# Optimization experiments

Measured on AMD Instinct MI355X. Metric: run time of the kernel, lower is better.

Reference implementation:

```python
import jax, jax.numpy as jnp
import numpy as np

M, D, NI, L, NPL, R, T = 2, 128, 131072, 4, 2048, 8, 32
N = NI + L * NPL  # total DAG nodes


def setup_inputs() -> dict:
    key = jax.random.key(0)
    ks = jax.random.split(key, 18)
    thax = jax.random.randint(ks[0], (NI,), 0, T)
    sine = jax.random.uniform(ks[1], (NI,), jnp.float32)
    # parents of layer-l deriv nodes index any node built earlier (topological)
    raw = jax.random.randint(ks[2], (L, NPL, 2), 0, 2**30)
    bounds = jnp.array([NI + l * NPL for l in range(L)])[:, None, None]
    par = raw % bounds
    ridx = jax.random.randint(ks[3], (L, NPL), 0, R)
    pos = jax.random.uniform(ks[4], (N,), jnp.float32) + 0.01
    neg = jax.random.uniform(ks[5], (N,), jnp.float32) + 0.01
    s = 0.05
    return {
        'thax': thax, 'sine': sine, 'par': par, 'ridx': ridx,
        'pos': pos, 'neg': neg,
        'init_table': jax.random.normal(ks[6], (M, T, D)) * s,
        's_vec': jax.random.normal(ks[7], (M, D)) * s,
        'W1': jax.random.normal(ks[8], (M, R, 2 * D, D)) * s,
        'b1': jax.random.normal(ks[9], (M, R, D)) * s,
        'W2': jax.random.normal(ks[10], (M, R, D, D)) * s,
        'b2': jax.random.normal(ks[11], (M, R, D)) * s,
        'tweaks': jax.random.normal(ks[12], (M, 1, 2)) * s,
        'We1': jax.random.normal(ks[13], (M, D, D)) * s,
        'be1': jax.random.normal(ks[14], (M, D)) * s,
        'we2': jax.random.normal(ks[15], (M, D)) * s,
        'be2': jax.random.normal(ks[16], (M,)) * s,
    }


def reference(thax, sine, par, ridx, pos, neg, init_table, s_vec,
              W1, b1, W2, b2, tweaks, We1, be1, we2, be2):
    # init nodes: thax embedding + sine embellishment (per model)
    emb0 = init_table[:, thax, :] + sine[None, :, None] * s_vec[:, None, :]  # [M,NI,D]
    store = jnp.zeros((M, N, D), emb0.dtype).at[:, :NI].set(emb0)
    # topological layers of deriv nodes: gather parents, rule-indexed 2-layer MLP
    for l in range(L):
        p, r = par[l], ridx[l]
        cat = store[:, p].reshape(M, NPL, 2 * D)               # gather parents
        h = jax.nn.relu(jnp.einsum('mnc,mncd->mnd', cat, W1[:, r]) + b1[:, r])
        out = (jnp.einsum('mnd,mnde->mne', h, W2[:, r]) + b2[:, r]
               + tweaks[:, 0, 1][:, None, None])
        store = store.at[:, NI + l * NPL: NI + (l + 1) * NPL].set(out)
    # eval_net: per-node scalar logit (+ per-problem tweak)
    he = jax.nn.relu(jnp.einsum('mnd,mde->mne', store, We1) + be1[:, None, :])
    logit = jnp.einsum('mnd,md->mn', he, we2) + be2[:, None] + tweaks[:, 0, 0][:, None]
    tot_pos, tot_neg = pos.sum(), neg.sum()
    pw = tot_neg / tot_pos  # POS_WEIGHT_EXTRA = 1.0
    gold = pos / (pos + neg)
    w = pos + neg
    # BCEWithLogitsLoss(pos_weight=pw) per node, weighted by (pos+neg)
    bce = -(pw * gold[None] * jax.nn.log_sigmoid(logit)
            + (1.0 - gold[None]) * jax.nn.log_sigmoid(-logit))
    loss = (w[None] * bce).sum(axis=1)                          # [M]
    posOK = jnp.where(logit >= 0, pos[None], 0.0).sum(axis=1)
    negOK = jnp.where(logit < 0, neg[None], 0.0).sum(axis=1)
    return (loss, posOK, negOK, tot_pos, tot_neg)
```

## Files before the change

kernel.cpp:

```cpp
#include <hip/hip_runtime.h>
#include <hip/hip_bf16.h>

#define M_ 2
#define D_ 128
#define NI_ 131072
#define L_ 4
#define NPL_ 2048
#define R_ 8
#define T_ 32
#define N_ (NI_ + L_ * NPL_)
#define ND_ (L_ * NPL_)
#define PSTRIDE_ 1792
#define PUSED_ 1665
#define FCAP_ 1280
#define SCAP_ 512
#define CCAP_ 24

typedef __bf16 bf16x8 __attribute__((ext_vector_type(8)));
typedef float f32x4 __attribute__((ext_vector_type(4)));
typedef unsigned short u16x4 __attribute__((ext_vector_type(4)));

#define OFF_W2T    0u
#define OFF_WE1T   524288u
#define OFF_TAB    589824u
#define OFF_SVEC   606208u
#define OFF_EA2    606720u
#define OFF_EWB    639488u
#define OFF_PA     641536u
#define OFF_PB     655872u
#define OFF_PPOK   670208u
#define OFF_PNOK   684544u
#define OFF_PTP    698880u
#define OFF_PTN    706048u
#define OFF_G      713216u
#define OFF_FLIST  1253888u
#define OFF_SLIST  1294848u
#define OFF_CFG    1296896u

__device__ __forceinline__ unsigned short f2bu(float f) {
  unsigned int u = __float_as_uint(f);
  u += 0x7fffu + ((u >> 16) & 1u);
  return (unsigned short)(u >> 16);
}
__device__ __forceinline__ float bfu2f(unsigned short u) {
  return __uint_as_float((unsigned int)u << 16);
}
__device__ __forceinline__ bf16x8 ldb8(const unsigned short* p) {
  return *reinterpret_cast<const bf16x8*>(p);
}

__global__ __launch_bounds__(256) void megaprep_kernel(
    const float* W1, const float* W2, const float* We1,
    const float* init_table, const float* s_vec,
    const float* b1, const float* be1, const float* we2,
    const int* ridx, const int* par,
    unsigned short* W2T, unsigned short* We1T,
    unsigned short* tab, unsigned short* svec,
    float* G, float* EA2, float* EWB,
    int* fastlist, int* slowlist, int* cfg, unsigned int* pzero) {
  __shared__ float smem[4352];
  __shared__ int lcnt;
  int job = blockIdx.x;
  int tid = threadIdx.x;

  if (job < 9) {
    int* out; int cap;
    if (job < 8) { out = fastlist + job * FCAP_; cap = FCAP_; }
    else         { out = slowlist;               cap = SCAP_; }
    if (tid == 0) lcnt = 0;
    __syncthreads();
    int lane = tid & 63;
    unsigned long long lmask_lt = (1ull << lane) - 1ull;
    for (int g = tid; g < ND_; g += 256) {
      int p0 = par[2 * g], p1 = par[2 * g + 1];
      bool fast = (p0 < NI_) && (p1 < NI_);
      bool match = (job < 8) ? (fast && ridx[g] == job) : (!fast);
      unsigned long long mask = __ballot(match);
      if (mask) {
        int leader = __ffsll((unsigned long long)mask) - 1;
        int pre = __popcll(mask & lmask_lt);
        int base_ = 0;
        if (lane == leader) base_ = atomicAdd(&lcnt, __popcll(mask));
        base_ = __shfl(base_, leader, 64);
        if (match) {
          int idx = base_ + pre;
          if (idx < cap) out[idx] = g;
        }
      }
    }
    __syncthreads();
    if (tid == 0) {
      int c = lcnt; if (c > cap) c = cap;
      cfg[job] = c;
    }
  } else if (job < 41) {
    int q = job - 9;
    int mr = q >> 1, slot = q & 1;
    int m = mr >> 3;
    for (int i = tid; i < 4352; i += 256) {
      int t = i >> 7, c = i & 127;
      smem[i] = (t < 32) ? init_table[(size_t)(m * T_ + t) * D_ + c]
              : (t == 32) ? s_vec[(size_t)m * D_ + c] : 0.f;
    }
    __syncthreads();
    int e = tid & 127, tg = tid >> 7;
    int t0 = tg ? 17 : 0;
    int nt = tg ? 16 : 17;
    float acc[17];
#pragma unroll
    for (int k = 0; k < 17; ++k) acc[k] = 0.f;
    const float* w1base = &W1[(size_t)(mr * 256 + slot * 128) * D_ + e];
#pragma unroll 4
    for (int c = 0; c < 128; ++c) {
      float w1c = w1base[(size_t)c * D_];
#pragma unroll
      for (int k = 0; k < 17; ++k)
        acc[k] = fmaf(smem[(t0 + k) * 128 + c], w1c, acc[k]);
    }
    float bb = b1[mr * D_ + e];
    for (int k = 0; k < nt; ++k) {
      int t = t0 + k;
      float v = acc[k];
      if (slot == 0 && t < 32) v += bb;
      G[((size_t)(mr * 2 + slot) * 33 + t) * D_ + e] = v;
    }
  } else if (job < 43) {
    int m = job - 41;
    for (int i = tid; i < 4352; i += 256) {
      int t = i >> 7, c = i & 127;
      smem[i] = (t < 32) ? init_table[(size_t)(m * T_ + t) * D_ + c]
              : (t == 32) ? s_vec[(size_t)m * D_ + c] : 0.f;
    }
    __syncthreads();
    int e = tid & 127, tg = tid >> 7;
    int t0 = tg ? 17 : 0;
    int nt = tg ? 16 : 17;
    float acc[17];
#pragma unroll
    for (int k = 0; k < 17; ++k) acc[k] = 0.f;
    const float* webase = &We1[(size_t)m * D_ * D_ + e];
#pragma unroll 4
    for (int c = 0; c < 128; ++c) {
      float wc = webase[(size_t)c * D_];
#pragma unroll
      for (int k = 0; k < 17; ++k)
        acc[k] = fmaf(smem[(t0 + k) * 128 + c], wc, acc[k]);
    }
    float bev = be1[m * D_ + e];
    for (int k = 0; k < nt; ++k) {
      int t = t0 + k;
      if (t < 32) {
        EA2[m * 4096 + ((e >> 1) * 32 + t) * 2 + (e & 1)] = acc[k] + bev;
      } else {
        EWB[(m * D_ + e) * 2 + 0] = acc[k];
        EWB[(m * D_ + e) * 2 + 1] = we2[m * D_ + e];
      }
    }
  } else if (job == 43) {
    for (int i = tid; i < 17920; i += 256) pzero[i] = 0u;
  } else if (job == 44) {
    for (int i = tid; i < 8448; i += 256) {
      if (i < 8192) tab[i] = f2bu(init_table[i]);
      else svec[i - 8192] = f2bu(s_vec[i - 8192]);
    }
  } else {
    int q0 = job - 45;
    const float* src; unsigned short* dst;
    int rblk, cblk;
    if (q0 < 256) {
      int z = q0 >> 4;
      src = W2 + (size_t)z * 16384; dst = W2T + (size_t)z * 16384;
      rblk = (q0 & 15) >> 2; cblk = q0 & 3;
    } else {
      int q = q0 - 256; int z = q >> 4;
      src = We1 + (size_t)z * 16384; dst = We1T + (size_t)z * 16384;
      rblk = (q & 15) >> 2; cblk = q & 3;
    }
    int r0 = rblk * 32, c0 = cblk * 32;
    float (*tile)[33] = (float(*)[33])smem;
    int tx = tid & 31, ty = tid >> 5;
#pragma unroll
    for (int k = 0; k < 4; ++k)
      tile[ty + 8 * k][tx] = src[(size_t)(r0 + ty + 8 * k) * D_ + c0 + tx];
    __syncthreads();
#pragma unroll
    for (int k = 0; k < 4; ++k)
      dst[(size_t)(c0 + ty + 8 * k) * D_ + r0 + tx] = f2bu(tile[tx][ty + 8 * k]);
  }
}

__global__ __launch_bounds__(256) void main_kernel(
    const int* thax, const float* sine, const int* par, const int* ridx,
    const float* pos, const float* neg,
    const float* W1, const float* b1, const float* b2, const float* tweaks,
    const float* G, const unsigned short* W2T, const unsigned short* We1T,
    const unsigned short* tab, const unsigned short* svec,
    const float* EA2, const float* EWB,
    const float* be1, const float* we2, const float* be2,
    const int* cfg, const int* fastlist, const int* slowlist,
    float* pA, float* pB, float* pPok, float* pNok, float* pTp, float* pTn) {
  __shared__ float sbuf[4448];
  int bid = blockIdx.x;
  int tid = threadIdx.x;
  int w = tid >> 6, lane = tid & 63;

  if (bid < 1024) {
    int m = bid >> 9, si = bid & 511;
    if (si >= cfg[8]) return;
    int*   list  = (int*)sbuf;
    int*   meta  = (int*)(sbuf + 24);
    unsigned short* catl = (unsigned short*)(sbuf + 32);
    float* hbuf  = sbuf + 160;
    float* hp0   = sbuf + 288;
    float* hp1   = sbuf + 416;
    unsigned short* cache = (unsigned short*)(sbuf + 544);

    int g_row = slowlist[si];
    if (tid == 0) {
      int nn = 0;
      list[nn++] = g_row;
      for (int i = 0; i < nn; ++i) {
        int g = list[i];
        for (int s = 0; s < 2; ++s) {
          int p = par[2 * g + s];
          if (p >= NI_) {
            int pg = p - NI_;
            bool found = false;
            for (int jj = 0; jj < nn; ++jj) if (list[jj] == pg) { found = true; break; }
            if (!found && nn < CCAP_) list[nn++] = pg;
          }
        }
      }
      for (int i = 1; i < nn; ++i) {
        int v = list[i]; int jj = i - 1;
        while (jj >= 0 && list[jj] > v) { list[jj + 1] = list[jj]; --jj; }
        list[jj + 1] = v;
      }
      meta[0] = nn;
    }
    __syncthreads();
    int NN = meta[0];
    float tw1 = tweaks[m * 2 + 1];
    for (int j = 0; j < NN; ++j) {
      int g = list[j];
      int r = ridx[g];
      int p0 = par[2 * g], p1 = par[2 * g + 1];
      bool fastn = (p0 < NI_) && (p1 < NI_);
      if (fastn) {
        if (tid < 128) {
          int d = tid;
          const float* Gm = &G[(size_t)(m * R_ + r) * 8448];
          float hv = Gm[thax[p0] * 128 + d] + Gm[(33 + thax[p1]) * 128 + d]
                   + sine[p0] * Gm[4096 + d] + sine[p1] * Gm[8320 + d];
          hbuf[d] = bfu2f(f2bu(fmaxf(hv, 0.f)));
        }
        __syncthreads();
      } else {
        if (tid == 0) {
          int s0 = -1, s1 = -1;
          if (p0 >= NI_) for (int jj = 0; jj < j; ++jj) if (list[jj] == p0 - NI_) { s0 = jj; break; }
          if (p1 >= NI_) for (int jj = 0; jj < j; ++jj) if (list[jj] == p1 - NI_) { s1 = jj; break; }
          meta[1] = s0; meta[2] = s1;
        }
        __syncthreads();
        {
          int c = tid; int p = (c < 128) ? p0 : p1; int cc = c & 127;
          int slot = (c < 128) ? meta[1] : meta[2];
          unsigned short v;
          if (p < NI_) {
            float tv = bfu2f(tab[(m * T_ + thax[p]) * D_ + cc])
                     + sine[p] * bfu2f(svec[m * D_ + cc]);
            v = f2bu(tv);
          } else {
            v = cache[slot * 128 + cc];
          }
          catl[c] = v;
        }
        __syncthreads();
        int d = tid & 127, half = tid >> 7;
        const float* w1r = &W1[(((size_t)(m * R_ + r)) * 256 + half * 128) * D_];
        float acc = 0.f;
#pragma unroll 8
        for (int c = 0; c < 128; ++c)
          acc = fmaf(bfu2f(catl[half * 128 + c]), w1r[(size_t)c * D_ + d], acc);
        if (half == 0) hp0[d] = acc; else hp1[d] = acc;
        __syncthreads();
        if (tid < 128) {
          float hv = b1[(m * R_ + r) * D_ + tid] + hp0[tid] + hp1[tid];
          hbuf[tid] = bfu2f(f2bu(fmaxf(hv, 0.f)));
        }
        __syncthreads();
      }
      {
        int e = tid & 127, half = tid >> 7;
        const u16x4* w2r4 = (const u16x4*)&W2T[((size_t)(m * R_ + r) * D_ + e) * D_ + half * 64];
        float acc = 0.f;
#pragma unroll
        for (int dd = 0; dd < 16; ++dd) {
          u16x4 wv = w2r4[dd];
          int db = half * 64 + dd * 4;
          acc = fmaf(bfu2f(wv[0]), hbuf[db + 0], acc);
          acc = fmaf(bfu2f(wv[1]), hbuf[db + 1], acc);
          acc = fmaf(bfu2f(wv[2]), hbuf[db + 2], acc);
          acc = fmaf(bfu2f(wv[3]), hbuf[db + 3], acc);
        }
        if (half == 0) hp0[e] = acc; else hp1[e] = acc;
      }
      __syncthreads();
      if (tid < 128) {
        float o = hp0[tid] + hp1[tid] + b2[(m * R_ + r) * D_ + tid] + tw1;
        cache[j * 128 + tid] = f2bu(o);
      }
      __syncthreads();
    }
    int jr = NN - 1;
    {
      int e = tid & 127, half = tid >> 7;
      const u16x4* wer4 = (const u16x4*)&We1T[((size_t)m * D_ + e) * D_ + half * 64];
      float acc = 0.f;
#pragma unroll
      for (int dd = 0; dd < 16; ++dd) {
        u16x4 wv = wer4[dd];
        int db = half * 64 + dd * 4;
        acc = fmaf(bfu2f(wv[0]), bfu2f(cache[jr * 128 + db + 0]), acc);
        acc = fmaf(bfu2f(wv[1]), bfu2f(cache[jr * 128 + db + 1]), acc);
        acc = fmaf(bfu2f(wv[2]), bfu2f(cache[jr * 128 + db + 2]), acc);
        acc = fmaf(bfu2f(wv[3]), bfu2f(cache[jr * 128 + db + 3]), acc);
      }
      if (half == 0) hp0[e] = acc; else hp1[e] = acc;
    }
    __syncthreads();
    if (tid < 128) {
      float he = hp0[tid] + hp1[tid] + be1[m * D_ + tid];
      he = he > 0.f ? he : 0.f;
      hbuf[tid] = he * we2[m * D_ + tid];
    }
    __syncthreads();
    if (tid < 64) {
      float s = hbuf[tid] + hbuf[tid + 64];
#pragma unroll
      for (int mask = 1; mask < 64; mask <<= 1) s += __shfl_xor(s, mask, 64);
      if (tid == 0) {
        float logit = s + be2[m] + tweaks[m * 2 + 0];
        int grow = NI_ + g_row;
        float p_ = pos[grow], n_ = neg[grow];
        float lse = log1pf(__expf(-fabsf(logit)));
        int slot = 1153 + si;
        pA[m * PSTRIDE_ + slot] = p_ * (fmaxf(-logit, 0.f) + lse);
        pB[m * PSTRIDE_ + slot] = n_ * (fmaxf(logit, 0.f) + lse);
        pPok[m * PSTRIDE_ + slot] = logit >= 0.f ? p_ : 0.f;
        pNok[m * PSTRIDE_ + slot] = logit < 0.f ? n_ : 0.f;
      }
    }
  } else if (bid < 2304) {
    int fb = bid - 1024;
    int m = fb / 640, q = fb % 640;
    int r = q / 80, tile = q % 80;
    int cnt = cfg[r];
    int base = tile * 16;
    if (base >= cnt) return;
    unsigned short* h_lds = (unsigned short*)sbuf;
    int*   t0a  = (int*)(sbuf + 1024);
    int*   t1a  = t0a + 16;
    float* s0a  = (float*)(t1a + 16);
    float* s1a  = s0a + 16;
    int*   gida = (int*)(s1a + 16);
    float* red2 = sbuf + 1104;
    if (tid < 16) {
      int loc = base + tid; if (loc >= cnt) loc = cnt - 1;
      int gid = fastlist[r * FCAP_ + loc];
      int p0 = par[2 * gid], p1 = par[2 * gid + 1];
      t0a[tid] = thax[p0]; s0a[tid] = sine[p0];
      t1a[tid] = thax[p1]; s1a[tid] = sine[p1];
      gida[tid] = gid;
    }
    __syncthreads();
    const float* Gm = &G[(size_t)(m * R_ + r) * 8448];
    {
      int row = tid >> 4, seg = tid & 15, d0 = seg * 8;
      int t0 = t0a[row], t1 = t1a[row];
      float s0 = s0a[row], s1 = s1a[row];
      const float* pa = &Gm[t0 * 128 + d0];
      const float* pb = &Gm[(33 + t1) * 128 + d0];
      const float* pu = &Gm[4096 + d0];
      const float* pv = &Gm[8320 + d0];
      bf16x8 hv;
#pragma unroll
      for (int half = 0; half < 2; ++half) {
        float4 a = *(const float4*)(pa + half * 4);
        float4 b = *(const float4*)(pb + half * 4);
        float4 u = *(const float4*)(pu + half * 4);
        float4 v = *(const float4*)(pv + half * 4);
        hv[half * 4 + 0] = (__bf16)fmaxf(a.x + b.x + s0 * u.x + s1 * v.x, 0.f);
        hv[half * 4 + 1] = (__bf16)fmaxf(a.y + b.y + s0 * u.y + s1 * v.y, 0.f);
        hv[half * 4 + 2] = (__bf16)fmaxf(a.z + b.z + s0 * u.z + s1 * v.z, 0.f);
        hv[half * 4 + 3] = (__bf16)fmaxf(a.w + b.w + s0 * u.w + s1 * v.w, 0.f);
      }
      *(bf16x8*)&h_lds[row * 128 + (d0 ^ ((row & 7) << 3))] = hv;
    }
    __syncthreads();
    int l15 = lane & 15, l4 = lane >> 4;
    const unsigned short* w2b = &W2T[(size_t)(m * R_ + r) * D_ * D_];
    f32x4 acc[2];
    acc[0] = (f32x4){0.f, 0.f, 0.f, 0.f};
    acc[1] = (f32x4){0.f, 0.f, 0.f, 0.f};
#pragma unroll
    for (int kc = 0; kc < 4; ++kc) {
      int d0 = kc * 32 + l4 * 8;
      bf16x8 a2 = ldb8(&h_lds[l15 * 128 + (d0 ^ ((l15 & 7) << 3))]);
#pragma unroll
      for (int f = 0; f < 2; ++f) {
        int fg = w * 2 + f;
        bf16x8 b = ldb8(&w2b[(fg * 16 + l15) * D_ + d0]);
        acc[f] = __builtin_amdgcn_mfma_f32_16x16x32_bf16(a2, b, acc[f], 0, 0, 0);
      }
    }
    float tw1 = tweaks[m * 2 + 1];
    const float* b2v = &b2[(m * R_ + r) * D_];
    __syncthreads();
#pragma unroll
    for (int i = 0; i < 4; ++i) {
      int row = l4 * 4 + i;
#pragma unroll
      for (int f = 0; f < 2; ++f) {
        int e = (w * 2 + f) * 16 + l15;
        h_lds[row * 128 + (e ^ ((row & 7) << 3))] = f2bu(acc[f][i] + b2v[e] + tw1);
      }
    }
    __syncthreads();
    f32x4 ae[2];
    ae[0] = (f32x4){0.f, 0.f, 0.f, 0.f};
    ae[1] = (f32x4){0.f, 0.f, 0.f, 0.f};
    const unsigned short* we1b = &We1T[(size_t)m * D_ * D_];
#pragma unroll
    for (int kc = 0; kc < 4; ++kc) {
      int d0 = kc * 32 + l4 * 8;
      bf16x8 a2 = ldb8(&h_lds[l15 * 128 + (d0 ^ ((l15 & 7) << 3))]);
#pragma unroll
      for (int f = 0; f < 2; ++f) {
        int fg = w * 2 + f;
        bf16x8 b = ldb8(&we1b[(fg * 16 + l15) * D_ + d0]);
        ae[f] = __builtin_amdgcn_mfma_f32_16x16x32_bf16(a2, b, ae[f], 0, 0, 0);
      }
    }
    float part[4] = {0.f, 0.f, 0.f, 0.f};
#pragma unroll
    for (int f = 0; f < 2; ++f) {
      int e = (w * 2 + f) * 16 + l15;
      float bb = be1[m * D_ + e];
      float wv = we2[m * D_ + e];
#pragma unroll
      for (int i = 0; i < 4; ++i) {
        float he = ae[f][i] + bb;
        he = he > 0.f ? he : 0.f;
        part[i] += he * wv;
      }
    }
#pragma unroll
    for (int mask = 1; mask < 16; mask <<= 1) {
#pragma unroll
      for (int i = 0; i < 4; ++i) part[i] += __shfl_xor(part[i], mask, 64);
    }
    if (l15 == 0) {
#pragma unroll
      for (int i = 0; i < 4; ++i) red2[w * 16 + l4 * 4 + i] = part[i];
    }
    __syncthreads();
    if (tid < 16) {
      int g = base + tid;
      float v6[4] = {0.f, 0.f, 0.f, 0.f};
      if (g < cnt) {
        float logit = red2[tid] + red2[16 + tid] + red2[32 + tid] + red2[48 + tid]
                    + be2[m] + tweaks[m * 2 + 0];
        int grow = NI_ + gida[tid];
        float p_ = pos[grow], n_ = neg[grow];
        float lse = log1pf(__expf(-fabsf(logit)));
        v6[0] = p_ * (fmaxf(-logit, 0.f) + lse);
        v6[1] = n_ * (fmaxf(logit, 0.f) + lse);
        v6[2] = logit >= 0.f ? p_ : 0.f;
        v6[3] = logit < 0.f ? n_ : 0.f;
      }
#pragma unroll
      for (int mask = 1; mask < 16; mask <<= 1) {
#pragma unroll
        for (int qq = 0; qq < 4; ++qq) v6[qq] += __shfl_xor(v6[qq], mask, 64);
      }
      if (tid == 0) {
        int slot = 512 + r * 80 + tile;
        pA[m * PSTRIDE_ + slot] = v6[0];
        pB[m * PSTRIDE_ + slot] = v6[1];
        pPok[m * PSTRIDE_ + slot] = v6[2];
        pNok[m * PSTRIDE_ + slot] = v6[3];
      }
    }
  } else if (bid < 3328) {
    int q = bid - 2304;
    int m = q >> 9, xb = q & 511;
    float* lea = sbuf;
    float* lwb = sbuf + 4096;
    float* red = sbuf + 4352;
    for (int i = tid; i < 4096; i += 256) lea[i] = EA2[m * 4096 + i];
    if (tid < 256) lwb[tid] = EWB[m * 256 + tid];
    __syncthreads();
    int row = xb * 256 + tid;
    int t = thax[row];
    float s = sine[row];
    float acc = 0.f;
#pragma unroll 8
    for (int p = 0; p < 64; ++p) {
      float2 ea = *(const float2*)&lea[(p * 32 + t) * 2];
      float4 wb = *(const float4*)&lwb[p * 4];
      float x0 = fmaf(s, wb.x, ea.x); x0 = fmaxf(x0, 0.f);
      acc = fmaf(x0, wb.y, acc);
      float x1 = fmaf(s, wb.z, ea.y); x1 = fmaxf(x1, 0.f);
      acc = fmaf(x1, wb.w, acc);
    }
    float logit = acc + be2[m] + tweaks[m * 2 + 0];
    float p_ = pos[row], n_ = neg[row];
    float lse = log1pf(__expf(-fabsf(logit)));
    float v[6];
    v[0] = p_ * (fmaxf(-logit, 0.f) + lse);
    v[1] = n_ * (fmaxf(logit, 0.f) + lse);
    v[2] = logit >= 0.f ? p_ : 0.f;
    v[3] = logit < 0.f ? n_ : 0.f;
    v[4] = p_; v[5] = n_;
#pragma unroll
    for (int mask = 1; mask < 64; mask <<= 1) {
#pragma unroll
      for (int k = 0; k < 6; ++k) v[k] += __shfl_xor(v[k], mask, 64);
    }
    if (lane == 0) {
#pragma unroll
      for (int k = 0; k < 6; ++k) red[k * 16 + w] = v[k];
    }
    __syncthreads();
    if (tid == 0) {
      float t6[6];
#pragma unroll
      for (int k = 0; k < 6; ++k)
        t6[k] = red[k * 16 + 0] + red[k * 16 + 1] + red[k * 16 + 2] + red[k * 16 + 3];
      pA[m * PSTRIDE_ + xb] = t6[0];
      pB[m * PSTRIDE_ + xb] = t6[1];
      pPok[m * PSTRIDE_ + xb] = t6[2];
      pNok[m * PSTRIDE_ + xb] = t6[3];
      if (m == 0) { pTp[xb] = t6[4]; pTn[xb] = t6[5]; }
    }
  } else {
    int j = bid - 3328;
    float* red = sbuf;
    const float* src = j ? neg : pos;
    float s = 0.f;
    for (int i = NI_ + tid; i < N_; i += 256) s += src[i];
#pragma unroll
    for (int mask = 1; mask < 64; mask <<= 1) s += __shfl_xor(s, mask, 64);
    if (lane == 0) red[w] = s;
    __syncthreads();
    if (tid == 0) {
      float t = red[0] + red[1] + red[2] + red[3];
      if (j == 0) pTp[1152] = t; else pTn[1152] = t;
    }
  }
}

__global__ __launch_bounds__(256) void finalize_kernel(
    const float* pA, const float* pB, const float* pPok, const float* pNok,
    const float* pTp, const float* pTn, float* out) {
  __shared__ float lred[10][4];
  const float* srcs[10] = {pA, pA + PSTRIDE_, pB, pB + PSTRIDE_,
                           pPok, pPok + PSTRIDE_, pNok, pNok + PSTRIDE_,
                           pTp, pTn};
  int tid = threadIdx.x;
  int w = tid >> 6, lane = tid & 63;
#pragma unroll
  for (int q = 0; q < 10; ++q) {
    float s = 0.f;
    for (int i = tid; i < PUSED_; i += 256) s += srcs[q][i];
#pragma unroll
    for (int mask = 1; mask < 64; mask <<= 1) s += __shfl_xor(s, mask, 64);
    if (lane == 0) lred[q][w] = s;
  }
  __syncthreads();
  if (tid == 0) {
    float totals[10];
#pragma unroll
    for (int q = 0; q < 10; ++q)
      totals[q] = lred[q][0] + lred[q][1] + lred[q][2] + lred[q][3];
    float tp = totals[8], tn = totals[9];
    float pw = tn / tp;
    out[0] = pw * totals[0] + totals[2];
    out[1] = pw * totals[1] + totals[3];
    out[2] = totals[4]; out[3] = totals[5];
    out[4] = totals[6]; out[5] = totals[7];
    out[6] = tp; out[7] = tn;
  }
}

extern "C" void kernel_launch(void* const* d_in, const int* in_sizes, int n_in,
                              void* d_out, int out_size, void* d_ws, size_t ws_size,
                              hipStream_t stream) {
  const int*   thax = (const int*)d_in[0];
  const float* sine = (const float*)d_in[1];
  const int*   par  = (const int*)d_in[2];
  const int*   ridx = (const int*)d_in[3];
  const float* pos  = (const float*)d_in[4];
  const float* neg  = (const float*)d_in[5];
  const float* init_table = (const float*)d_in[6];
  const float* s_vec = (const float*)d_in[7];
  const float* W1 = (const float*)d_in[8];
  const float* b1 = (const float*)d_in[9];
  const float* W2 = (const float*)d_in[10];
  const float* b2 = (const float*)d_in[11];
  const float* tweaks = (const float*)d_in[12];
  const float* We1 = (const float*)d_in[13];
  const float* be1 = (const float*)d_in[14];
  const float* we2 = (const float*)d_in[15];
  const float* be2 = (const float*)d_in[16];

  char* ws = (char*)d_ws;
  unsigned short* W2T  = (unsigned short*)(ws + OFF_W2T);
  unsigned short* We1T = (unsigned short*)(ws + OFF_WE1T);
  unsigned short* tab  = (unsigned short*)(ws + OFF_TAB);
  unsigned short* svec = (unsigned short*)(ws + OFF_SVEC);
  float* EA2  = (float*)(ws + OFF_EA2);
  float* EWB  = (float*)(ws + OFF_EWB);
  float* pA   = (float*)(ws + OFF_PA);
  float* pB   = (float*)(ws + OFF_PB);
  float* pPok = (float*)(ws + OFF_PPOK);
  float* pNok = (float*)(ws + OFF_PNOK);
  float* pTp  = (float*)(ws + OFF_PTP);
  float* pTn  = (float*)(ws + OFF_PTN);
  float* G    = (float*)(ws + OFF_G);
  int* fastlist = (int*)(ws + OFF_FLIST);
  int* slowlist = (int*)(ws + OFF_SLIST);
  int* cfg      = (int*)(ws + OFF_CFG);

  megaprep_kernel<<<333, 256, 0, stream>>>(
      W1, W2, We1, init_table, s_vec, b1, be1, we2, ridx, par,
      W2T, We1T, tab, svec, G, EA2, EWB,
      fastlist, slowlist, cfg, (unsigned int*)pA);
  main_kernel<<<3330, 256, 0, stream>>>(
      thax, sine, par, ridx, pos, neg, W1, b1, b2, tweaks,
      G, W2T, We1T, tab, svec, EA2, EWB, be1, we2, be2,
      cfg, fastlist, slowlist,
      pA, pB, pPok, pNok, pTp, pTn);
  finalize_kernel<<<1, 256, 0, stream>>>(pA, pB, pPok, pNok, pTp, pTn,
                                         (float*)d_out);
}
```

Measured before the change: 88.57 us.

## Split node classification into per-layer compaction blocks and per-layer slow regions

The list-building stage that scanned all derived nodes in 9 blocks is split into 35 blocks, each scanning one 2048-node layer (32 fast lists by rule and layer, 3 slow lists for layers 1-3). The main kernel's slow-path and fast-path block indexing is remapped to these per-layer lists, and the partials buffer stride is enlarged to match. This shortens the serial scan in the prep kernel and spreads compaction over more CUs, but launches more main-kernel blocks, many of which exit early. The unroll factor on the W1/We1 precompute loops also goes from 4 to 8.

```diff
diff --git a/kernel.cpp b/kernel.cpp
--- a/kernel.cpp
+++ b/kernel.cpp
@@ -10,10 +10,10 @@
 #define T_ 32
 #define N_ (NI_ + L_ * NPL_)
 #define ND_ (L_ * NPL_)
-#define PSTRIDE_ 1792
-#define PUSED_ 1665
-#define FCAP_ 1280
-#define SCAP_ 512
+#define PSTRIDE_ 2048
+#define PUSED_ 1921
+#define FCAP_ 320
+#define SCAP_ 256
 #define CCAP_ 24
 
 typedef __bf16 bf16x8 __attribute__((ext_vector_type(8)));
@@ -27,15 +27,15 @@
 #define OFF_EA2    606720u
 #define OFF_EWB    639488u
 #define OFF_PA     641536u
-#define OFF_PB     655872u
-#define OFF_PPOK   670208u
-#define OFF_PNOK   684544u
-#define OFF_PTP    698880u
-#define OFF_PTN    706048u
-#define OFF_G      713216u
-#define OFF_FLIST  1253888u
-#define OFF_SLIST  1294848u
-#define OFF_CFG    1296896u
+#define OFF_PB     657920u
+#define OFF_PPOK   674304u
+#define OFF_PNOK   690688u
+#define OFF_PTP    707072u
+#define OFF_PTN    715264u
+#define OFF_G      723456u
+#define OFF_FLIST  1264128u
+#define OFF_SLIST  1305088u
+#define OFF_CFG    1308160u
 
 __device__ __forceinline__ unsigned short f2bu(float f) {
   unsigned int u = __float_as_uint(f);
@@ -63,18 +63,25 @@
   int job = blockIdx.x;
   int tid = threadIdx.x;
 
-  if (job < 9) {
-    int* out; int cap;
-    if (job < 8) { out = fastlist + job * FCAP_; cap = FCAP_; }
-    else         { out = slowlist;               cap = SCAP_; }
+  if (job < 35) {
+    int* out; int cap; int g0, g1; int rr = -1;
+    if (job < 32) {
+      rr = job >> 2; int quarter = job & 3;
+      out = fastlist + job * FCAP_; cap = FCAP_;
+      g0 = quarter * 2048; g1 = g0 + 2048;
+    } else {
+      int l = job - 31;
+      out = slowlist + (job - 32) * SCAP_; cap = SCAP_;
+      g0 = l * 2048; g1 = g0 + 2048;
+    }
     if (tid == 0) lcnt = 0;
     __syncthreads();
     int lane = tid & 63;
     unsigned long long lmask_lt = (1ull << lane) - 1ull;
-    for (int g = tid; g < ND_; g += 256) {
+    for (int g = g0 + tid; g < g1; g += 256) {
       int p0 = par[2 * g], p1 = par[2 * g + 1];
       bool fast = (p0 < NI_) && (p1 < NI_);
-      bool match = (job < 8) ? (fast && ridx[g] == job) : (!fast);
+      bool match = (job < 32) ? (fast && ridx[g] == rr) : (!fast);
       unsigned long long mask = __ballot(match);
       if (mask) {
         int leader = __ffsll((unsigned long long)mask) - 1;
@@ -93,8 +100,8 @@
       int c = lcnt; if (c > cap) c = cap;
       cfg[job] = c;
     }
-  } else if (job < 41) {
-    int q = job - 9;
+  } else if (job < 67) {
+    int q = job - 35;
     int mr = q >> 1, slot = q & 1;
     int m = mr >> 3;
     for (int i = tid; i < 4352; i += 256) {
@@ -110,7 +117,7 @@
 #pragma unroll
     for (int k = 0; k < 17; ++k) acc[k] = 0.f;
     const float* w1base = &W1[(size_t)(mr * 256 + slot * 128) * D_ + e];
-#pragma unroll 4
+#pragma unroll 8
     for (int c = 0; c < 128; ++c) {
       float w1c = w1base[(size_t)c * D_];
 #pragma unroll
@@ -124,8 +131,8 @@
       if (slot == 0 && t < 32) v += bb;
       G[((size_t)(mr * 2 + slot) * 33 + t) * D_ + e] = v;
     }
-  } else if (job < 43) {
-    int m = job - 41;
+  } else if (job < 69) {
+    int m = job - 67;
     for (int i = tid; i < 4352; i += 256) {
       int t = i >> 7, c = i & 127;
       smem[i] = (t < 32) ? init_table[(size_t)(m * T_ + t) * D_ + c]
@@ -139,7 +146,7 @@
 #pragma unroll
     for (int k = 0; k < 17; ++k) acc[k] = 0.f;
     const float* webase = &We1[(size_t)m * D_ * D_ + e];
-#pragma unroll 4
+#pragma unroll 8
     for (int c = 0; c < 128; ++c) {
       float wc = webase[(size_t)c * D_];
 #pragma unroll
@@ -156,15 +163,15 @@
         EWB[(m * D_ + e) * 2 + 1] = we2[m * D_ + e];
       }
     }
-  } else if (job == 43) {
-    for (int i = tid; i < 17920; i += 256) pzero[i] = 0u;
-  } else if (job == 44) {
+  } else if (job == 69) {
+    for (int i = tid; i < 20480; i += 256) pzero[i] = 0u;
+  } else if (job == 70) {
     for (int i = tid; i < 8448; i += 256) {
       if (i < 8192) tab[i] = f2bu(init_table[i]);
       else svec[i - 8192] = f2bu(s_vec[i - 8192]);
     }
   } else {
-    int q0 = job - 45;
+    int q0 = job - 71;
     const float* src; unsigned short* dst;
     int rblk, cblk;
     if (q0 < 256) {
@@ -204,9 +211,11 @@
   int tid = threadIdx.x;
   int w = tid >> 6, lane = tid & 63;
 
-  if (bid < 1024) {
-    int m = bid >> 9, si = bid & 511;
-    if (si >= cfg[8]) return;
+  if (bid < 1536) {
+    int m = (bid >= 768) ? 1 : 0;
+    int si = bid - m * 768;
+    int region = si >> 8, idx = si & 255;
+    if (idx >= cfg[32 + region]) return;
     int*   list  = (int*)sbuf;
     int*   meta  = (int*)(sbuf + 24);
     unsigned short* catl = (unsigned short*)(sbuf + 32);
@@ -215,7 +224,7 @@
     float* hp1   = sbuf + 416;
     unsigned short* cache = (unsigned short*)(sbuf + 544);
 
-    int g_row = slowlist[si];
+    int g_row = slowlist[region * SCAP_ + idx];
     if (tid == 0) {
       int nn = 0;
       list[nn++] = g_row;
@@ -352,11 +361,12 @@
         pNok[m * PSTRIDE_ + slot] = logit < 0.f ? n_ : 0.f;
       }
     }
-  } else if (bid < 2304) {
-    int fb = bid - 1024;
+  } else if (bid < 2816) {
+    int fb = bid - 1536;
     int m = fb / 640, q = fb % 640;
-    int r = q / 80, tile = q % 80;
-    int cnt = cfg[r];
+    int vr = q / 20, tile = q % 20;
+    int r = vr >> 2;
+    int cnt = cfg[vr];
     int base = tile * 16;
     if (base >= cnt) return;
     unsigned short* h_lds = (unsigned short*)sbuf;
@@ -368,7 +378,7 @@
     float* red2 = sbuf + 1104;
     if (tid < 16) {
       int loc = base + tid; if (loc >= cnt) loc = cnt - 1;
-      int gid = fastlist[r * FCAP_ + loc];
+      int gid = fastlist[vr * FCAP_ + loc];
       int p0 = par[2 * gid], p1 = par[2 * gid + 1];
       t0a[tid] = thax[p0]; s0a[tid] = sine[p0];
       t1a[tid] = thax[p1]; s1a[tid] = sine[p1];
@@ -486,15 +496,15 @@
         for (int qq = 0; qq < 4; ++qq) v6[qq] += __shfl_xor(v6[qq], mask, 64);
       }
       if (tid == 0) {
-        int slot = 512 + r * 80 + tile;
+        int slot = 512 + vr * 20 + tile;
         pA[m * PSTRIDE_ + slot] = v6[0];
         pB[m * PSTRIDE_ + slot] = v6[1];
         pPok[m * PSTRIDE_ + slot] = v6[2];
         pNok[m * PSTRIDE_ + slot] = v6[3];
       }
     }
-  } else if (bid < 3328) {
-    int q = bid - 2304;
+  } else if (bid < 3840) {
+    int q = bid - 2816;
     int m = q >> 9, xb = q & 511;
     float* lea = sbuf;
     float* lwb = sbuf + 4096;
@@ -546,7 +556,7 @@
       if (m == 0) { pTp[xb] = t6[4]; pTn[xb] = t6[5]; }
     }
   } else {
-    int j = bid - 3328;
+    int j = bid - 3840;
     float* red = sbuf;
     const float* src = j ? neg : pos;
     float s = 0.f;
@@ -634,11 +644,11 @@
   int* slowlist = (int*)(ws + OFF_SLIST);
   int* cfg      = (int*)(ws + OFF_CFG);
 
-  megaprep_kernel<<<333, 256, 0, stream>>>(
+  megaprep_kernel<<<359, 256, 0, stream>>>(
       W1, W2, We1, init_table, s_vec, b1, be1, we2, ridx, par,
       W2T, We1T, tab, svec, G, EA2, EWB,
       fastlist, slowlist, cfg, (unsigned int*)pA);
-  main_kernel<<<3330, 256, 0, stream>>>(
+  main_kernel<<<3842, 256, 0, stream>>>(
       thax, sine, par, ridx, pos, neg, W1, b1, b2, tweaks,
       G, W2T, We1T, tab, svec, EA2, EWB, be1, we2, be2,
       cfg, fastlist, slowlist,
```

After: 115.2 us. 30.0% more time.
